# Optimization experiments

Measured on AMD Instinct MI355X. Metric: run time of the kernel, lower is better.

Reference implementation:

```python
import jax, jax.numpy as jnp
import numpy as np

D_MODEL = 1024
NUM_HEADS = 16
HEAD_DIM = D_MODEL // NUM_HEADS


def setup_inputs() -> dict:
    key = jax.random.key(0)
    ks = jax.random.split(key, 5)
    B, S = 2, 2048
    x = jax.random.normal(ks[0], (B, S, D_MODEL), dtype=jnp.float32)
    Wq = jax.random.normal(ks[1], (D_MODEL, D_MODEL), dtype=jnp.float32) * 0.02
    Wk = jax.random.normal(ks[2], (D_MODEL, D_MODEL), dtype=jnp.float32) * 0.02
    Wv = jax.random.normal(ks[3], (D_MODEL, D_MODEL), dtype=jnp.float32) * 0.02
    Wo = jax.random.normal(ks[4], (D_MODEL, D_MODEL), dtype=jnp.float32) * 0.02
    return {"x": x, "Wq": Wq, "Wk": Wk, "Wv": Wv, "Wo": Wo}


def reference(x, Wq, Wk, Wv, Wo):
    B, S, _ = x.shape
    # QKV projections (Linear is x @ W, no bias)
    q = (x @ Wq).reshape(B, S, NUM_HEADS, HEAD_DIM).transpose(0, 2, 1, 3)  # [B,H,S,Dh]
    k = (x @ Wk).reshape(B, S, NUM_HEADS, HEAD_DIM).transpose(0, 2, 1, 3)
    v = (x @ Wv).reshape(B, S, NUM_HEADS, HEAD_DIM).transpose(0, 2, 1, 3)
    scale = 1.0 / jnp.sqrt(jnp.asarray(HEAD_DIM, dtype=x.dtype))
    scores = jnp.einsum("bhqd,bhkd->bhqk", q, k) * scale  # [B,H,S,S]
    causal = jnp.tril(jnp.ones((S, S), dtype=bool))
    scores = jnp.where(causal, scores, -jnp.inf)
    probs = jax.nn.softmax(scores, axis=-1)
    out = jnp.einsum("bhqk,bhkd->bhqd", probs, v)  # [B,H,S,Dh]
    out = out.transpose(0, 2, 1, 3).reshape(B, S, D_MODEL)
    return out @ Wo
```

## Files before the change

### kernel.cpp

```cpp
#include <hip/hip_runtime.h>

typedef __attribute__((ext_vector_type(4))) short short4v;
typedef __attribute__((ext_vector_type(8))) short short8v;
typedef __attribute__((ext_vector_type(4))) float float4v;
typedef __attribute__((ext_vector_type(4))) int int4v;

#define GLD_LDS16(gsrc, ldst)                                                             \
    __builtin_amdgcn_global_load_lds(                                                     \
        (const __attribute__((address_space(1))) void*)(gsrc),                            \
        (__attribute__((address_space(3))) void*)(ldst), 16, 0, 0)

__device__ __forceinline__ short f2bf(float f) {
    unsigned u = __builtin_bit_cast(unsigned, f);
    u += 0x7fffu + ((u >> 16) & 1u);
    return (short)(u >> 16);
}

__global__ void k_prep(const float* __restrict__ x, short* __restrict__ xb,
                       const float* __restrict__ W0, const float* __restrict__ W1,
                       const float* __restrict__ W2, const float* __restrict__ W3,
                       short* __restrict__ Wt) {
    __shared__ float tile[32][33];
    int bid = blockIdx.x;
    if (bid < 4096) {
        int i = bid * 256 + threadIdx.x;
        float4v v = ((const float4v*)x)[i];
        short4v o;
        o[0] = f2bf(v[0]); o[1] = f2bf(v[1]); o[2] = f2bf(v[2]); o[3] = f2bf(v[3]);
        ((short4v*)xb)[i] = o;
        return;
    }
    int L = bid - 4096;
    int z = L >> 10;
    int xy = L & 1023;
    int bx = xy & 31, by = xy >> 5;
    const float* W = z == 0 ? W0 : z == 1 ? W1 : z == 2 ? W2 : W3;
    short* dst = Wt + (size_t)z * 1024 * 1024;
    int x0 = bx * 32, y0 = by * 32;
    int tx = threadIdx.x & 31, ty = threadIdx.x >> 5;
#pragma unroll
    for (int j = 0; j < 4; j++) {
        int r = ty + j * 8;
        tile[r][tx] = W[(size_t)(y0 + r) * 1024 + x0 + tx];
    }
    __syncthreads();
#pragma unroll
    for (int j = 0; j < 4; j++) {
        int r = ty + j * 8;
        dst[(size_t)(x0 + r) * 1024 + y0 + tx] = f2bf(tile[tx][r]);
    }
}

__launch_bounds__(512, 4)
__global__ void k_gemmQKV(const short* __restrict__ A, const short* __restrict__ Wtb,
                          short* __restrict__ Qb, short* __restrict__ Kb,
                          short* __restrict__ Vtb) {
    __shared__ short As[2][128][64];
    __shared__ short Bs[2][128][64];
    int t = threadIdx.x;
    int l = t & 63, w = t >> 6;
    int wm = w >> 2, wn = w & 3;
    int lr = l & 15, lg = l >> 4;
    int m0 = blockIdx.x * 128;
    int nfull = blockIdx.y * 128;
    int which = nfull >> 10;
    int nb = nfull & 1023;

    int srow = l >> 3;
    int sg = (l & 7) ^ srow;
    const short* Ab0 = A + (size_t)(m0 + w * 8 + srow) * 1024 + sg * 8;
    const short* Ab1 = Ab0 + 64 * 1024;
    const short* Bb0 = Wtb + (size_t)(nfull + w * 8 + srow) * 1024 + sg * 8;
    const short* Bb1 = Bb0 + 64 * 1024;

    float4v acc[4][2] = {};

#define STAGE(bb, k0)                                   \
    do {                                                \
        GLD_LDS16(Ab0 + (k0), &As[bb][w * 8][0]);       \
        GLD_LDS16(Ab1 + (k0), &As[bb][64 + w * 8][0]);  \
        GLD_LDS16(Bb0 + (k0), &Bs[bb][w * 8][0]);       \
        GLD_LDS16(Bb1 + (k0), &Bs[bb][64 + w * 8][0]);  \
    } while (0)

    STAGE(0, 0);
    __syncthreads();
    int cur = 0;

    if (which == 2) {
        for (int kt = 0; kt < 16; kt++) {
            if (kt + 1 < 16) STAGE(cur ^ 1, (kt + 1) * 64);
#pragma unroll
            for (int ks = 0; ks < 2; ks++) {
                short8v af[4], bfv[2];
                int hh = ks * 4 + lg;
                int sw = ((hh ^ (lr & 7)) * 8);
#pragma unroll
                for (int fm = 0; fm < 4; fm++)
                    af[fm] = *(const short8v*)&As[cur][wm * 64 + fm * 16 + lr][sw];
#pragma unroll
                for (int fn = 0; fn < 2; fn++)
                    bfv[fn] = *(const short8v*)&Bs[cur][wn * 32 + fn * 16 + lr][sw];
                __builtin_amdgcn_s_setprio(1);
#pragma unroll
                for (int fm = 0; fm < 4; fm++)
#pragma unroll
                    for (int fn = 0; fn < 2; fn++)
                        acc[fm][fn] = __builtin_amdgcn_mfma_f32_16x16x32_bf16(bfv[fn], af[fm], acc[fm][fn], 0, 0, 0);
                __builtin_amdgcn_s_setprio(0);
            }
            __syncthreads();
            cur ^= 1;
        }
    } else {
        for (int kt = 0; kt < 16; kt++) {
            if (kt + 1 < 16) STAGE(cur ^ 1, (kt + 1) * 64);
#pragma unroll
            for (int ks = 0; ks < 2; ks++) {
                short8v af[4], bfv[2];
                int hh = ks * 4 + lg;
                int sw = ((hh ^ (lr & 7)) * 8);
#pragma unroll
                for (int fm = 0; fm < 4; fm++)
                    af[fm] = *(const short8v*)&As[cur][wm * 64 + fm * 16 + lr][sw];
#pragma unroll
                for (int fn = 0; fn < 2; fn++)
                    bfv[fn] = *(const short8v*)&Bs[cur][wn * 32 + fn * 16 + lr][sw];
                __builtin_amdgcn_s_setprio(1);
#pragma unroll
                for (int fm = 0; fm < 4; fm++)
#pragma unroll
                    for (int fn = 0; fn < 2; fn++)
                        acc[fm][fn] = __builtin_amdgcn_mfma_f32_16x16x32_bf16(af[fm], bfv[fn], acc[fm][fn], 0, 0, 0);
                __builtin_amdgcn_s_setprio(0);
            }
            __syncthreads();
            cur ^= 1;
        }
    }
#undef STAGE

    if (which < 2) {
        short* out = (which == 0) ? Qb : Kb;
        float scale = (which == 0) ? 0.125f * 1.44269504088896f : 1.0f;
#pragma unroll
        for (int fm = 0; fm < 4; fm++)
#pragma unroll
            for (int fn = 0; fn < 2; fn++)
#pragma unroll
                for (int r = 0; r < 4; r++) {
                    int m = m0 + wm * 64 + fm * 16 + lg * 4 + r;
                    int n = nb + wn * 32 + fn * 16 + lr;
                    float v = acc[fm][fn][r] * scale;
                    int b = m >> 11, s = m & 2047, h = n >> 6, dh = n & 63;
                    out[(((size_t)(b * 16 + h)) * 2048 + s) * 64 + dh] = f2bf(v);
                }
    } else {
#pragma unroll
        for (int fm = 0; fm < 4; fm++)
#pragma unroll
            for (int fn = 0; fn < 2; fn++)
#pragma unroll
                for (int r = 0; r < 4; r++) {
                    int n = nb + wn * 32 + fn * 16 + lg * 4 + r;
                    int m = m0 + wm * 64 + fm * 16 + lr;
                    int b = m >> 11, s = m & 2047, h = n >> 6, dh = n & 63;
                    Vtb[(((size_t)(b * 16 + h)) * 64 + dh) * 2048 + s] = f2bf(acc[fm][fn][r]);
                }
    }
}

__launch_bounds__(512, 4)
__global__ void k_gemmO(const short* __restrict__ A, const short* __restrict__ Bt,
                        float* __restrict__ outF) {
    __shared__ short As[2][128][64];
    __shared__ short Bs[2][128][64];
    int t = threadIdx.x;
    int l = t & 63, w = t >> 6;
    int wm = w >> 2, wn = w & 3;
    int lr = l & 15, lg = l >> 4;
    int m0 = blockIdx.x * 128, n0 = blockIdx.y * 128;

    int srow = l >> 3;
    int sg = (l & 7) ^ srow;
    const short* Ab0 = A + (size_t)(m0 + w * 8 + srow) * 1024 + sg * 8;
    const short* Ab1 = Ab0 + 64 * 1024;
    const short* Bb0 = Bt + (size_t)(n0 + w * 8 + srow) * 1024 + sg * 8;
    const short* Bb1 = Bb0 + 64 * 1024;

    float4v acc[4][2] = {};

#define STAGE(bb, k0)                                   \
    do {                                                \
        GLD_LDS16(Ab0 + (k0), &As[bb][w * 8][0]);       \
        GLD_LDS16(Ab1 + (k0), &As[bb][64 + w * 8][0]);  \
        GLD_LDS16(Bb0 + (k0), &Bs[bb][w * 8][0]);       \
        GLD_LDS16(Bb1 + (k0), &Bs[bb][64 + w * 8][0]);  \
    } while (0)

    STAGE(0, 0);
    __syncthreads();
    int cur = 0;

    for (int kt = 0; kt < 16; kt++) {
        if (kt + 1 < 16) STAGE(cur ^ 1, (kt + 1) * 64);
#pragma unroll
        for (int ks = 0; ks < 2; ks++) {
            short8v af[4], bfv[2];
            int hh = ks * 4 + lg;
            int sw = ((hh ^ (lr & 7)) * 8);
#pragma unroll
            for (int fm = 0; fm < 4; fm++)
                af[fm] = *(const short8v*)&As[cur][wm * 64 + fm * 16 + lr][sw];
#pragma unroll
            for (int fn = 0; fn < 2; fn++)
                bfv[fn] = *(const short8v*)&Bs[cur][wn * 32 + fn * 16 + lr][sw];
            __builtin_amdgcn_s_setprio(1);
#pragma unroll
            for (int fm = 0; fm < 4; fm++)
#pragma unroll
                for (int fn = 0; fn < 2; fn++)
                    acc[fm][fn] = __builtin_amdgcn_mfma_f32_16x16x32_bf16(af[fm], bfv[fn], acc[fm][fn], 0, 0, 0);
            __builtin_amdgcn_s_setprio(0);
        }
        __syncthreads();
        cur ^= 1;
    }
#undef STAGE

#pragma unroll
    for (int fm = 0; fm < 4; fm++)
#pragma unroll
        for (int fn = 0; fn < 2; fn++)
#pragma unroll
            for (int r = 0; r < 4; r++) {
                int m = m0 + wm * 64 + fm * 16 + lg * 4 + r;
                int n = n0 + wn * 32 + fn * 16 + lr;
                outF[(size_t)m * 1024 + n] = acc[fm][fn][r];
            }
}

__launch_bounds__(256, 2)
__global__ void k_attn(const short* __restrict__ Qb, const short* __restrict__ Kb,
                       const short* __restrict__ Vtb, short* __restrict__ Ob) {
    __shared__ short K_lds[2][64][64];
    __shared__ short V_lds[2][64][64];
    __shared__ short p_lds[4][2][16][64];
    int t = threadIdx.x;
    int l = t & 63, w = t >> 6;
    int lr = l & 15, lg = l >> 4;

    int L = blockIdx.x;
    int bh = L & 31;
    int g = L >> 5;
    int p = (g < 8) ? g : 23 - g;
    int nch = 32 - p;

    const short* Qp = Qb + (size_t)bh * 2048 * 64;
    const short* Kp = Kb + (size_t)bh * 2048 * 64;
    const short* Vp = Vtb + (size_t)bh * 64 * 2048;

    auto stage = [&](int bb, int kv0) {
#pragma unroll
        for (int i = 0; i < 2; i++) {
            int s = t + i * 256;
            int row = s >> 3, cg = s & 7;
            int cs = (cg ^ (row & 7)) * 8;
            GLD_LDS16(&Kp[(size_t)(kv0 + row) * 64 + cs], (short*)K_lds[bb] + (size_t)s * 8);
            GLD_LDS16(&Vp[(size_t)row * 2048 + kv0 + cs], (short*)V_lds[bb] + (size_t)s * 8);
        }
    };

    stage(0, 0);

    int q0a = (31 - p) * 64 + w * 16;
    int q0b = p * 64 + w * 16;
    short8v qf0a = *(const short8v*)&Qp[(size_t)(q0a + lr) * 64 + lg * 8];
    short8v qf1a = *(const short8v*)&Qp[(size_t)(q0a + lr) * 64 + 32 + lg * 8];
    short8v qf0b = *(const short8v*)&Qp[(size_t)(q0b + lr) * 64 + lg * 8];
    short8v qf1b = *(const short8v*)&Qp[(size_t)(q0b + lr) * 64 + 32 + lg * 8];

    float4v oa[4] = {}, ob[4] = {};
    float mra = -3e38f, mrb = -3e38f;
    float lsa = 0.f, lsb = 0.f;
    int cur = 0;
    int b = bh >> 4, h = bh & 15;

    auto softmax_store = [&](float4v (&s)[4], float& mr, float& ls,
                             float4v (&o)[4], int X) {
        float mx = -3e38f;
#pragma unroll
        for (int t4 = 0; t4 < 4; t4++)
#pragma unroll
            for (int r = 0; r < 4; r++) mx = fmaxf(mx, s[t4][r]);

        if (!__all(mx - mr <= 8.f)) {
            float m_ = fmaxf(mx, __shfl_xor(mx, 16));
            m_ = fmaxf(m_, __shfl_xor(m_, 32));
            float mnew = fmaxf(mr, m_);
            float sc = __builtin_amdgcn_exp2f(mr - mnew);
            mr = mnew;
            ls *= sc;
#pragma unroll
            for (int r = 0; r < 4; r++) {
                float scq = __shfl(sc, lg * 4 + r);
                o[0][r] *= scq; o[1][r] *= scq; o[2][r] *= scq; o[3][r] *= scq;
            }
        }
        int rx = lr & 7;
        int half = (lg & 1) * 4;
#pragma unroll
        for (int t4 = 0; t4 < 4; t4++) {
            float e0 = __builtin_amdgcn_exp2f(s[t4][0] - mr);
            float e1 = __builtin_amdgcn_exp2f(s[t4][1] - mr);
            float e2 = __builtin_amdgcn_exp2f(s[t4][2] - mr);
            float e3 = __builtin_amdgcn_exp2f(s[t4][3] - mr);
            ls += (e0 + e1) + (e2 + e3);
            unsigned lo, hi;
            asm("v_cvt_pk_bf16_f32 %0, %1, %2" : "=v"(lo) : "v"(e0), "v"(e1));
            asm("v_cvt_pk_bf16_f32 %0, %1, %2" : "=v"(hi) : "v"(e2), "v"(e3));
            int grp = (2 * t4 + (lg >> 1)) ^ rx;
            *(unsigned long long*)&p_lds[w][X][lr][grp * 8 + half] =
                (unsigned long long)lo | ((unsigned long long)hi << 32);
        }
    };

    __syncthreads();

    for (int ci = 0; ci < nch; ci++) {
        int kv0 = ci * 64;
        bool dual = (ci <= p);

        if (ci + 1 < nch) stage(cur ^ 1, (ci + 1) * 64);

        const short* Kf = (const short*)K_lds[cur];
        float4v sa[4] = {}, sb[4] = {};
        __builtin_amdgcn_s_setprio(1);
#pragma unroll
        for (int t4 = 0; t4 < 4; t4++) {
            int krow = t4 * 16 + lr;
            int sw = (krow & 7);
            short8v kfa = *(const short8v*)&Kf[krow * 64 + ((lg ^ sw) * 8)];
            short8v kfb = *(const short8v*)&Kf[krow * 64 + (((lg ^ 4) ^ sw) * 8)];
            sa[t4] = __builtin_amdgcn_mfma_f32_16x16x32_bf16(kfa, qf0a, sa[t4], 0, 0, 0);
            sa[t4] = __builtin_amdgcn_mfma_f32_16x16x32_bf16(kfb, qf1a, sa[t4], 0, 0, 0);
            if (dual) {
                sb[t4] = __builtin_amdgcn_mfma_f32_16x16x32_bf16(kfa, qf0b, sb[t4], 0, 0, 0);
                sb[t4] = __builtin_amdgcn_mfma_f32_16x16x32_bf16(kfb, qf1b, sb[t4], 0, 0, 0);
            }
        }
        __builtin_amdgcn_s_setprio(0);

        if (kv0 + 63 > q0a) {
#pragma unroll
            for (int t4 = 0; t4 < 4; t4++)
#pragma unroll
                for (int r = 0; r < 4; r++)
                    if (kv0 + t4 * 16 + 4 * lg + r > q0a + lr) sa[t4][r] = -3e38f;
        }
        if (dual && kv0 + 63 > q0b) {
#pragma unroll
            for (int t4 = 0; t4 < 4; t4++)
#pragma unroll
                for (int r = 0; r < 4; r++)
                    if (kv0 + t4 * 16 + 4 * lg + r > q0b + lr) sb[t4][r] = -3e38f;
        }

        softmax_store(sa, mra, lsa, oa, 0);
        if (dual) softmax_store(sb, mrb, lsb, ob, 1);

        int prx = lr & 7;
        short8v pa0 = *(const short8v*)&p_lds[w][0][lr][8 * (lg ^ prx)];
        short8v pa1 = *(const short8v*)&p_lds[w][0][lr][8 * ((4 + lg) ^ prx)];
        short8v pb0, pb1;
        if (dual) {
            pb0 = *(const short8v*)&p_lds[w][1][lr][8 * (lg ^ prx)];
            pb1 = *(const short8v*)&p_lds[w][1][lr][8 * ((4 + lg) ^ prx)];
        }

        const short* Vf = (const short*)V_lds[cur];
        __builtin_amdgcn_s_setprio(1);
#pragma unroll
        for (int dt = 0; dt < 4; dt++) {
            int vrow = dt * 16 + lr;
            int sw = (vrow & 7);
            short8v vfa = *(const short8v*)&Vf[vrow * 64 + ((lg ^ sw) * 8)];
            short8v vfb = *(const short8v*)&Vf[vrow * 64 + (((lg ^ 4) ^ sw) * 8)];
            oa[dt] = __builtin_amdgcn_mfma_f32_16x16x32_bf16(pa0, vfa, oa[dt], 0, 0, 0);
            oa[dt] = __builtin_amdgcn_mfma_f32_16x16x32_bf16(pa1, vfb, oa[dt], 0, 0, 0);
            if (dual) {
                ob[dt] = __builtin_amdgcn_mfma_f32_16x16x32_bf16(pb0, vfa, ob[dt], 0, 0, 0);
                ob[dt] = __builtin_amdgcn_mfma_f32_16x16x32_bf16(pb1, vfb, ob[dt], 0, 0, 0);
            }
        }
        __builtin_amdgcn_s_setprio(0);

        __syncthreads();
        cur ^= 1;
    }

    float la = lsa, lb = lsb;
    la += __shfl_xor(la, 16); la += __shfl_xor(la, 32);
    lb += __shfl_xor(lb, 16); lb += __shfl_xor(lb, 32);
    float inva_ = 1.0f / la, invb_ = 1.0f / lb;
    float inva[4], invb[4];
#pragma unroll
    for (int r = 0; r < 4; r++) {
        inva[r] = __shfl(inva_, lg * 4 + r);
        invb[r] = __shfl(invb_, lg * 4 + r);
    }
#pragma unroll
    for (int dt = 0; dt < 4; dt++)
#pragma unroll
        for (int r = 0; r < 4; r++) {
            int qa = q0a + lg * 4 + r;
            int qb = q0b + lg * 4 + r;
            Ob[((size_t)(b * 2048 + qa)) * 1024 + h * 64 + dt * 16 + lr] = f2bf(oa[dt][r] * inva[r]);
            Ob[((size_t)(b * 2048 + qb)) * 1024 + h * 64 + dt * 16 + lr] = f2bf(ob[dt][r] * invb[r]);
        }
}

extern "C" void kernel_launch(void* const* d_in, const int* in_sizes, int n_in,
                              void* d_out, int out_size, void* d_ws, size_t ws_size,
                              hipStream_t stream) {
    const float* x  = (const float*)d_in[0];
    const float* Wq = (const float*)d_in[1];
    const float* Wk = (const float*)d_in[2];
    const float* Wv = (const float*)d_in[3];
    const float* Wo = (const float*)d_in[4];
    float* out = (float*)d_out;

    char* ws = (char*)d_ws;
    short* xb  = (short*)(ws);
    short* Wtb = (short*)(ws + 8388608);
    short* Qb  = (short*)(ws + 16777216);
    short* Kb  = (short*)(ws + 25165824);
    short* Vtb = (short*)(ws + 33554432);
    short* Ob  = (short*)(ws + 41943040);

    k_prep<<<8192, 256, 0, stream>>>(x, xb, Wq, Wk, Wv, Wo, Wtb);
    k_gemmQKV<<<dim3(32, 24), 512, 0, stream>>>(xb, Wtb, Qb, Kb, Vtb);
    k_attn<<<512, 256, 0, stream>>>(Qb, Kb, Vtb, Ob);
    k_gemmO<<<dim3(32, 8), 512, 0, stream>>>(Ob, Wtb + 3 * 1048576, out);
}
```

Before: 106.8 us.

## Keep softmax probabilities in registers instead of LDS round-trip for PV MFMA

Drops the per-warp LDS buffer that held the bf16 probabilities. The P operand for the PV MFMA is now packed directly from the score accumulator registers. To keep the k-index mapping consistent, the V fragment loads are rearranged to gather four short4 pieces per pair of MFMAs instead of two short8 loads. This removes LDS writes and reads and the shared memory footprint per step, in exchange for more, narrower V LDS reads and some register shuffling.

```diff
diff --git a/kernel.cpp b/kernel.cpp
--- a/kernel.cpp
+++ b/kernel.cpp
@@ -245,7 +245,6 @@
                        const short* __restrict__ Vtb, short* __restrict__ Ob) {
     __shared__ short K_lds[2][64][64];
     __shared__ short V_lds[2][64][64];
-    __shared__ short p_lds[4][2][16][64];
     int t = threadIdx.x;
     int l = t & 63, w = t >> 6;
     int lr = l & 15, lg = l >> 4;
@@ -285,9 +284,11 @@
     float lsa = 0.f, lsb = 0.f;
     int cur = 0;
     int b = bh >> 4, h = bh & 15;
-
-    auto softmax_store = [&](float4v (&s)[4], float& mr, float& ls,
-                             float4v (&o)[4], int X) {
+    int g0 = lg >> 1;
+    int hb = (lg & 1) * 4;
+
+    auto softmax_pack = [&](float4v (&s)[4], float& mr, float& ls, float4v (&o)[4],
+                            short8v& pa0, short8v& pa1) {
         float mx = -3e38f;
 #pragma unroll
         for (int t4 = 0; t4 < 4; t4++)
@@ -307,8 +308,7 @@
                 o[0][r] *= scq; o[1][r] *= scq; o[2][r] *= scq; o[3][r] *= scq;
             }
         }
-        int rx = lr & 7;
-        int half = (lg & 1) * 4;
+        unsigned d[8];
 #pragma unroll
         for (int t4 = 0; t4 < 4; t4++) {
             float e0 = __builtin_amdgcn_exp2f(s[t4][0] - mr);
@@ -316,13 +316,11 @@
             float e2 = __builtin_amdgcn_exp2f(s[t4][2] - mr);
             float e3 = __builtin_amdgcn_exp2f(s[t4][3] - mr);
             ls += (e0 + e1) + (e2 + e3);
-            unsigned lo, hi;
-            asm("v_cvt_pk_bf16_f32 %0, %1, %2" : "=v"(lo) : "v"(e0), "v"(e1));
-            asm("v_cvt_pk_bf16_f32 %0, %1, %2" : "=v"(hi) : "v"(e2), "v"(e3));
-            int grp = (2 * t4 + (lg >> 1)) ^ rx;
-            *(unsigned long long*)&p_lds[w][X][lr][grp * 8 + half] =
-                (unsigned long long)lo | ((unsigned long long)hi << 32);
-        }
+            asm("v_cvt_pk_bf16_f32 %0, %1, %2" : "=v"(d[2 * t4])     : "v"(e0), "v"(e1));
+            asm("v_cvt_pk_bf16_f32 %0, %1, %2" : "=v"(d[2 * t4 + 1]) : "v"(e2), "v"(e3));
+        }
+        pa0 = __builtin_bit_cast(short8v, int4v{(int)d[0], (int)d[1], (int)d[2], (int)d[3]});
+        pa1 = __builtin_bit_cast(short8v, int4v{(int)d[4], (int)d[5], (int)d[6], (int)d[7]});
     };
 
     __syncthreads();
@@ -366,17 +364,9 @@
                     if (kv0 + t4 * 16 + 4 * lg + r > q0b + lr) sb[t4][r] = -3e38f;
         }
 
-        softmax_store(sa, mra, lsa, oa, 0);
-        if (dual) softmax_store(sb, mrb, lsb, ob, 1);
-
-        int prx = lr & 7;
-        short8v pa0 = *(const short8v*)&p_lds[w][0][lr][8 * (lg ^ prx)];
-        short8v pa1 = *(const short8v*)&p_lds[w][0][lr][8 * ((4 + lg) ^ prx)];
-        short8v pb0, pb1;
-        if (dual) {
-            pb0 = *(const short8v*)&p_lds[w][1][lr][8 * (lg ^ prx)];
-            pb1 = *(const short8v*)&p_lds[w][1][lr][8 * ((4 + lg) ^ prx)];
-        }
+        short8v pa0, pa1, pb0, pb1;
+        softmax_pack(sa, mra, lsa, oa, pa0, pa1);
+        if (dual) softmax_pack(sb, mrb, lsb, ob, pb0, pb1);
 
         const short* Vf = (const short*)V_lds[cur];
         __builtin_amdgcn_s_setprio(1);
@@ -384,8 +374,16 @@
         for (int dt = 0; dt < 4; dt++) {
             int vrow = dt * 16 + lr;
             int sw = (vrow & 7);
-            short8v vfa = *(const short8v*)&Vf[vrow * 64 + ((lg ^ sw) * 8)];
-            short8v vfb = *(const short8v*)&Vf[vrow * 64 + (((lg ^ 4) ^ sw) * 8)];
+            const short* Vr = Vf + vrow * 64;
+            short4v a0 = *(const short4v*)&Vr[((g0    ) ^ sw) * 8 + hb];
+            short4v a1 = *(const short4v*)&Vr[((g0 + 2) ^ sw) * 8 + hb];
+            short4v b0 = *(const short4v*)&Vr[((g0 + 4) ^ sw) * 8 + hb];
+            short4v b1 = *(const short4v*)&Vr[((g0 + 6) ^ sw) * 8 + hb];
+            short8v vfa, vfb;
+            vfa[0] = a0[0]; vfa[1] = a0[1]; vfa[2] = a0[2]; vfa[3] = a0[3];
+            vfa[4] = a1[0]; vfa[5] = a1[1]; vfa[6] = a1[2]; vfa[7] = a1[3];
+            vfb[0] = b0[0]; vfb[1] = b0[1]; vfb[2] = b0[2]; vfb[3] = b0[3];
+            vfb[4] = b1[0]; vfb[5] = b1[1]; vfb[6] = b1[2]; vfb[7] = b1[3];
             oa[dt] = __builtin_amdgcn_mfma_f32_16x16x32_bf16(pa0, vfa, oa[dt], 0, 0, 0);
             oa[dt] = __builtin_amdgcn_mfma_f32_16x16x32_bf16(pa1, vfb, oa[dt], 0, 0, 0);
             if (dual) {
```

Result: no change. 105.2 us (median of 3 runs) (-1.5%).
